# Kernel optimization log

Measured on AMD Instinct MI355X. Metric: run time of the kernel, lower is better.

Reference implementation:

```python
import jax, jax.numpy as jnp
import numpy as np

N, E = 50000, 600000
IN_C, HID, OUT_C = 256, 128, 2
R, B, L = 7, 8, 3
ALPHA = 0.1


def _rgcn(x, src, dst, etype, comp, basis, root, bias):
    # comp: [R,B], basis: [B,d,d] -> per-relation weights W: [R,d,d]
    n, d = x.shape
    W = jnp.einsum('rb,bdf->rdf', comp, basis)
    # combined (dst, relation) segment id for per-relation mean aggregation
    seg = dst * R + etype
    msg = x[src]  # [E,d] gather
    s = jax.ops.segment_sum(msg, seg, num_segments=n * R)  # [N*R,d]
    cnt = jax.ops.segment_sum(jnp.ones((E,), x.dtype), seg, num_segments=n * R)
    agg = (s / jnp.maximum(cnt, 1.0)[:, None]).reshape(n, R, d)  # per-relation mean
    return x @ root + bias + jnp.einsum('nrd,rdf->nf', agg, W)


def setup_inputs() -> dict:
    key = jax.random.key(0)
    ks = jax.random.split(key, 10)
    sc = 0.05
    x = jax.random.normal(ks[0], (N, IN_C), dtype=jnp.float32)
    edge_index = jax.random.randint(ks[1], (2, E), 0, N)
    edge_type = jax.random.randint(ks[2], (E,), 0, R)
    # GPR temp init: alpha*(1-alpha)^k, last entry (1-alpha)^K
    temp = jnp.asarray(ALPHA * (1.0 - ALPHA) ** np.arange(L + 1), dtype=jnp.float32)
    temp = temp.at[-1].set((1.0 - ALPHA) ** L)
    lin1_w = jax.random.normal(ks[3], (IN_C, HID), jnp.float32) * sc
    lin1_b = jnp.zeros((HID,), jnp.float32)
    lin2_w = jax.random.normal(ks[4], (HID, OUT_C), jnp.float32) * sc
    lin2_b = jnp.zeros((OUT_C,), jnp.float32)
    comps = jax.random.normal(ks[5], (L, R, B), jnp.float32) * sc
    bases = jax.random.normal(ks[6], (L, B, HID, HID), jnp.float32) * sc
    roots = jax.random.normal(ks[7], (L, HID, HID), jnp.float32) * sc
    conv_biases = jnp.zeros((L, HID), jnp.float32)
    return dict(x=x, edge_index=edge_index, edge_type=edge_type, temp=temp,
                lin1_w=lin1_w, lin1_b=lin1_b, lin2_w=lin2_w, lin2_b=lin2_b,
                comps=comps, bases=bases, roots=roots, conv_biases=conv_biases)


def reference(x, edge_index, edge_type, temp, lin1_w, lin1_b, lin2_w, lin2_b,
              comps, bases, roots, conv_biases):
    src, dst = edge_index[0], edge_index[1]
    h = x @ lin1_w + lin1_b
    hidden = h * temp[0]
    cur = hidden
    for i in range(L):
        cur = _rgcn(cur, src, dst, edge_type, comps[i], bases[i], roots[i], conv_biases[i])
        if i < L - 1:
            cur = jax.nn.relu(cur)  # dropout p=0.4 is identity in eval mode
        hidden = hidden + temp[i + 1] * cur
    return hidden @ lin2_w + lin2_b
```

## Files before the change

### kernel.cpp

```cpp
#include <hip/hip_runtime.h>
#include <cstdint>


constexpr int N_NODES  = 50000;
constexpr int E_EDGES  = 600000;
constexpr int R_REL    = 7;
constexpr int HID      = 128;
constexpr int IN_C     = 256;
constexpr int L_LAYERS = 3;
constexpr int AGG_COLS = 896;
constexpr int K_CAT    = 1024;
constexpr int SCAN_BLOCKS = (N_NODES + 255) / 256;

#define DEVI __device__ __forceinline__

using short8  = __attribute__((ext_vector_type(8))) short;
using floatx4 = __attribute__((ext_vector_type(4))) float;

DEVI unsigned short f2bf(float f) {
  unsigned u = __float_as_uint(f);
  unsigned r = (u + 0x7FFFu + ((u >> 16) & 1u)) >> 16;
  return (unsigned short)r;
}
DEVI float bf2f(unsigned short h) { return __uint_as_float(((unsigned)h) << 16); }

__global__ __launch_bounds__(256) void cast_x_kernel(
    const float* __restrict__ x, unsigned short* __restrict__ xbf)
{
  int i = blockIdx.x * 256 + threadIdx.x;
  if (i >= N_NODES * IN_C / 4) return;
  float4 v = ((const float4*)x)[i];
  uint2 p;
  p.x = (unsigned)f2bf(v.x) | ((unsigned)f2bf(v.y) << 16);
  p.y = (unsigned)f2bf(v.z) | ((unsigned)f2bf(v.w) << 16);
  ((uint2*)xbf)[i] = p;
}

__global__ __launch_bounds__(256) void cast_w1_kernel(
    const float* __restrict__ w1, unsigned short* __restrict__ w1T)
{
  int t = blockIdx.x * 256 + threadIdx.x;
  if (t >= HID * IN_C) return;
  int m = t >> 8, k = t & 255;
  w1T[m * IN_C + k] = f2bf(w1[k * HID + m]);
}

__global__ __launch_bounds__(256) void build_wcat2(
    const float* __restrict__ comps,
    const float* __restrict__ bases,
    const float* __restrict__ roots,
    unsigned short* __restrict__ wcat2T)
{
  int t = blockIdx.x * 256 + threadIdx.x;
  if (t >= L_LAYERS * 128 * K_CAT) return;
  int l   = t >> 17;
  int rem = t & 131071;
  int f   = rem >> 10;
  int k   = rem & 1023;
  float v;
  if (k < 128) {
    v = roots[((size_t)l * 128 + k) * 128 + f];
  } else {
    int r = (k - 128) >> 7, d = (k - 128) & 127;
    const float* cp = comps + ((size_t)l * R_REL + r) * 8;
    const float* bp = bases + (((size_t)l * 8) * 128 + d) * 128 + f;
    float s = 0.f;
#pragma unroll
    for (int b = 0; b < 8; ++b) s += cp[b] * bp[(size_t)b * 128 * 128];
    v = s;
  }
  wcat2T[t] = f2bf(v);
}

__global__ __launch_bounds__(256) void hist_kernel(
    const int* __restrict__ ei, const int* __restrict__ et,
    int* __restrict__ cntRel, int* __restrict__ cntDst)
{
  int e = blockIdx.x * 256 + threadIdx.x;
  if (e >= E_EDGES) return;
  int dst = ei[E_EDGES + e];
  atomicAdd(&cntRel[dst * R_REL + et[e]], 1);
  atomicAdd(&cntDst[dst], 1);
}

__global__ __launch_bounds__(256) void inv_kernel(float* __restrict__ invc)
{
  int s = blockIdx.x * 256 + threadIdx.x;
  if (s >= N_NODES * R_REL) return;
  int c = ((const int*)invc)[s];
  if (c < 1) c = 1;
  invc[s] = 1.0f / (float)c;
}

__global__ __launch_bounds__(256) void scan1_kernel(
    const int* __restrict__ cntDst, int* __restrict__ tmpOff,
    int* __restrict__ blockSums)
{
  __shared__ int s[256];
  int i = blockIdx.x * 256 + threadIdx.x;
  int v = (i < N_NODES) ? cntDst[i] : 0;
  s[threadIdx.x] = v;
  __syncthreads();
#pragma unroll
  for (int d = 1; d < 256; d <<= 1) {
    int t = (threadIdx.x >= d) ? s[threadIdx.x - d] : 0;
    __syncthreads();
    s[threadIdx.x] += t;
    __syncthreads();
  }
  if (i < N_NODES) tmpOff[i] = s[threadIdx.x] - v;
  if (threadIdx.x == 255) blockSums[blockIdx.x] = s[255];
}

__global__ __launch_bounds__(256) void scan2_kernel(int* __restrict__ blockSums)
{
  __shared__ int s[256];
  int v = (threadIdx.x < SCAN_BLOCKS) ? blockSums[threadIdx.x] : 0;
  s[threadIdx.x] = v;
  __syncthreads();
#pragma unroll
  for (int d = 1; d < 256; d <<= 1) {
    int t = (threadIdx.x >= d) ? s[threadIdx.x - d] : 0;
    __syncthreads();
    s[threadIdx.x] += t;
    __syncthreads();
  }
  if (threadIdx.x < SCAN_BLOCKS) blockSums[threadIdx.x] = s[threadIdx.x] - v;
}

__global__ __launch_bounds__(256) void scan3_kernel(
    const int* __restrict__ tmpOff, const int* __restrict__ blockSums,
    int* __restrict__ dstStart)
{
  int i = blockIdx.x * 256 + threadIdx.x;
  if (i < N_NODES) dstStart[i] = tmpOff[i] + blockSums[blockIdx.x];
  if (i == 0) dstStart[N_NODES] = E_EDGES;
}

__global__ __launch_bounds__(256) void place_kernel(
    const int* __restrict__ ei, const int* __restrict__ et,
    const int* __restrict__ dstStart, int* __restrict__ cursor,
    int* __restrict__ epack)
{
  int e = blockIdx.x * 256 + threadIdx.x;
  if (e >= E_EDGES) return;
  int src = ei[e], dst = ei[E_EDGES + e], r = et[e];
  int pos = dstStart[dst] + atomicAdd(&cursor[dst], 1);
  epack[pos] = src | (r << 16);
}

__global__ __launch_bounds__(256) void agg2_kernel(
    const unsigned short* __restrict__ curA,
    const int* __restrict__ epack,
    const int* __restrict__ dstStart,
    const float* __restrict__ invc,
    unsigned short* __restrict__ aggB)
{
  __shared__ float accF[4][AGG_COLS];
  const int tid  = threadIdx.x;
  const int w    = tid >> 6;
  const int lane = tid & 63;
  const int dst0 = blockIdx.x * 4;
  const int dst  = dst0 + w;

  for (int i = tid; i < 4 * AGG_COLS; i += 256) ((float*)accF)[i] = 0.f;
  __syncthreads();

  int p0 = dstStart[dst], p1 = dstStart[dst + 1];
  for (int p = p0; p < p1; p += 64) {
    int m = p1 - p; if (m > 64) m = 64;
    int pk_l = (lane < m) ? epack[p + lane] : 0;
    for (int i = 0; i < m; ++i) {
      int pk  = __shfl(pk_l, i);
      int src = pk & 0xFFFF;
      int r   = pk >> 16;
      unsigned v = *(const unsigned*)(curA + (size_t)src * HID + lane * 2);
      float2* ap = (float2*)&accF[w][r * HID + lane * 2];
      float2 a = *ap;
      a.x += bf2f((unsigned short)(v & 0xFFFF));
      a.y += bf2f((unsigned short)(v >> 16));
      *ap = a;
    }
  }
  __syncthreads();

  for (int c = tid; c < 4 * (AGG_COLS / 8); c += 256) {
    int dl  = c / 112;
    int cin = c - dl * 112;
    int d0  = cin * 8;
    int r   = d0 >> 7;
    float sc = invc[(dst0 + dl) * R_REL + r];
    const float* ap = &accF[dl][d0];
    uint4 pck;
    pck.x = (unsigned)f2bf(ap[0] * sc) | ((unsigned)f2bf(ap[1] * sc) << 16);
    pck.y = (unsigned)f2bf(ap[2] * sc) | ((unsigned)f2bf(ap[3] * sc) << 16);
    pck.z = (unsigned)f2bf(ap[4] * sc) | ((unsigned)f2bf(ap[5] * sc) << 16);
    pck.w = (unsigned)f2bf(ap[6] * sc) | ((unsigned)f2bf(ap[7] * sc) << 16);
    *(uint4*)(aggB + (size_t)(dst0 + dl) * AGG_COLS + d0) = pck;
  }
}

__global__ __launch_bounds__(256) void gemm_lin1(
    const unsigned short* __restrict__ A,
    const unsigned short* __restrict__ BT,
    const float* __restrict__ bias,
    const float* __restrict__ temp,
    float* __restrict__ out0,
    unsigned short* __restrict__ outT)
{
  __shared__ unsigned short As[128][136];
  __shared__ unsigned short Bs[128][136];
  const int tid  = threadIdx.x;
  const int row0 = blockIdx.x * 128;
  const int lane = tid & 63;
  const int wid  = tid >> 6;
  const int wrow = (wid & 1) * 64;
  const int wcol = (wid >> 1) * 64;
  const int l15  = lane & 15;
  const int quad = lane >> 4;

  floatx4 acc[4][4] = {};

  for (int k0 = 0; k0 < IN_C; k0 += 128) {
#pragma unroll
    for (int it = 0; it < 8; ++it) {
      int chunk = it * 256 + tid;
      int r = chunk >> 4, cc = (chunk & 15) << 3;
      int grow = row0 + r;
      uint4 va = make_uint4(0u, 0u, 0u, 0u);
      if (grow < N_NODES)
        va = *(const uint4*)(A + (size_t)grow * IN_C + k0 + cc);
      *(uint4*)(&As[r][cc]) = va;
      *(uint4*)(&Bs[r][cc]) = *(const uint4*)(BT + (size_t)r * IN_C + k0 + cc);
    }
    __syncthreads();
#pragma unroll
    for (int ks = 0; ks < 4; ++ks) {
      int kc = ks * 32 + quad * 8;
      short8 af[4], bfr[4];
#pragma unroll
      for (int i = 0; i < 4; ++i)
        af[i] = *(const short8*)(&As[wrow + i * 16 + l15][kc]);
#pragma unroll
      for (int j = 0; j < 4; ++j)
        bfr[j] = *(const short8*)(&Bs[wcol + j * 16 + l15][kc]);
#pragma unroll
      for (int i = 0; i < 4; ++i)
#pragma unroll
        for (int j = 0; j < 4; ++j)
          acc[i][j] = __builtin_amdgcn_mfma_f32_16x16x32_bf16(
              af[i], bfr[j], acc[i][j], 0, 0, 0);
    }
    __syncthreads();
  }

  float t0 = temp[0];
#pragma unroll
  for (int i = 0; i < 4; ++i) {
    int lrow0 = wrow + i * 16 + quad * 4;
#pragma unroll
    for (int j = 0; j < 4; ++j) {
      int gcol = wcol + j * 16 + l15;
      float bb = bias[gcol];
#pragma unroll
      for (int r = 0; r < 4; ++r) {
        float v = t0 * (acc[i][j][r] + bb);
        int grow = row0 + lrow0 + r;
        if (grow < N_NODES) out0[(size_t)grow * HID + gcol] = v;
        As[lrow0 + r][gcol] = f2bf(v);
      }
    }
  }
  __syncthreads();
#pragma unroll
  for (int it = 0; it < 8; ++it) {
    int chunk = it * 256 + tid;
    int r = chunk >> 4, cc = (chunk & 15) << 3;
    int grow = row0 + r;
    if (grow < N_NODES)
      *(uint4*)(outT + (size_t)grow * HID + cc) = *(const uint4*)(&As[r][cc]);
  }
}

__global__ __launch_bounds__(256) void gemm_layer(
    const unsigned short* __restrict__ curA,
    const unsigned short* __restrict__ aggB,
    const unsigned short* __restrict__ BT,
    const float* __restrict__ bias,
    float* __restrict__ out0)
{
  __shared__ unsigned short As[128][136];
  __shared__ unsigned short Bs[128][136];
  const int tid  = threadIdx.x;
  const int row0 = blockIdx.x * 128;
  const int lane = tid & 63;
  const int wid  = tid >> 6;
  const int wrow = (wid & 1) * 64;
  const int wcol = (wid >> 1) * 64;
  const int l15  = lane & 15;
  const int quad = lane >> 4;

  floatx4 acc[4][4] = {};

  for (int k0 = 0; k0 < K_CAT; k0 += 128) {
#pragma unroll
    for (int it = 0; it < 8; ++it) {
      int chunk = it * 256 + tid;
      int r = chunk >> 4, cc = (chunk & 15) << 3;
      int grow = row0 + r;
      uint4 va = make_uint4(0u, 0u, 0u, 0u);
      if (grow < N_NODES) {
        if (k0 == 0)
          va = *(const uint4*)(curA + (size_t)grow * HID + cc);
        else
          va = *(const uint4*)(aggB + (size_t)grow * AGG_COLS + (k0 - 128) + cc);
      }
      *(uint4*)(&As[r][cc]) = va;
      *(uint4*)(&Bs[r][cc]) = *(const uint4*)(BT + (size_t)r * K_CAT + k0 + cc);
    }
    __syncthreads();
#pragma unroll
    for (int ks = 0; ks < 4; ++ks) {
      int kc = ks * 32 + quad * 8;
      short8 af[4], bfr[4];
#pragma unroll
      for (int i = 0; i < 4; ++i)
        af[i] = *(const short8*)(&As[wrow + i * 16 + l15][kc]);
#pragma unroll
      for (int j = 0; j < 4; ++j)
        bfr[j] = *(const short8*)(&Bs[wcol + j * 16 + l15][kc]);
#pragma unroll
      for (int i = 0; i < 4; ++i)
#pragma unroll
        for (int j = 0; j < 4; ++j)
          acc[i][j] = __builtin_amdgcn_mfma_f32_16x16x32_bf16(
              af[i], bfr[j], acc[i][j], 0, 0, 0);
    }
    __syncthreads();
  }

#pragma unroll
  for (int i = 0; i < 4; ++i) {
    int lrow0 = wrow + i * 16 + quad * 4;
#pragma unroll
    for (int j = 0; j < 4; ++j) {
      int gcol = wcol + j * 16 + l15;
      float bb = bias[gcol];
#pragma unroll
      for (int r = 0; r < 4; ++r) {
        int grow = row0 + lrow0 + r;
        if (grow < N_NODES)
          out0[(size_t)grow * HID + gcol] = acc[i][j][r] + bb;
      }
    }
  }
}

__global__ __launch_bounds__(256) void epilogue_kernel(
    const float* __restrict__ curB, float* __restrict__ hidden,
    unsigned short* __restrict__ curA, const float* __restrict__ temp, int layer)
{
  int i = blockIdx.x * 256 + threadIdx.x;
  if (i >= N_NODES * HID / 4) return;
  float tl = temp[layer + 1];
  float4 c = ((const float4*)curB)[i];
  if (layer < L_LAYERS - 1) {
    c.x = fmaxf(c.x, 0.f); c.y = fmaxf(c.y, 0.f);
    c.z = fmaxf(c.z, 0.f); c.w = fmaxf(c.w, 0.f);
  }
  float4 h = ((const float4*)hidden)[i];
  h.x += tl * c.x; h.y += tl * c.y; h.z += tl * c.z; h.w += tl * c.w;
  ((float4*)hidden)[i] = h;
  if (layer < L_LAYERS - 1) {
    uint2 p;
    p.x = (unsigned)f2bf(c.x) | ((unsigned)f2bf(c.y) << 16);
    p.y = (unsigned)f2bf(c.z) | ((unsigned)f2bf(c.w) << 16);
    ((uint2*)curA)[i] = p;
  }
}

__global__ __launch_bounds__(256) void final_kernel(
    const float* __restrict__ hidden, const float* __restrict__ w2,
    const float* __restrict__ b2, float* __restrict__ out)
{
  int node = blockIdx.x * 4 + (threadIdx.x >> 6);
  int lane = threadIdx.x & 63;
  if (node >= N_NODES) return;
  float h0 = hidden[(size_t)node * HID + lane];
  float h1 = hidden[(size_t)node * HID + 64 + lane];
  float a0 = h0 * w2[lane * 2 + 0] + h1 * w2[(lane + 64) * 2 + 0];
  float a1 = h0 * w2[lane * 2 + 1] + h1 * w2[(lane + 64) * 2 + 1];
#pragma unroll
  for (int off = 32; off > 0; off >>= 1) {
    a0 += __shfl_down(a0, off);
    a1 += __shfl_down(a1, off);
  }
  if (lane == 0) {
    out[node * 2 + 0] = a0 + b2[0];
    out[node * 2 + 1] = a1 + b2[1];
  }
}

extern "C" void kernel_launch(void* const* d_in, const int* in_sizes, int n_in,
                              void* d_out, int out_size, void* d_ws, size_t ws_size,
                              hipStream_t stream) {
  const float* x     = (const float*)d_in[0];
  const int*   ei    = (const int*)d_in[1];
  const int*   et    = (const int*)d_in[2];
  const float* temp  = (const float*)d_in[3];
  const float* w1    = (const float*)d_in[4];
  const float* b1    = (const float*)d_in[5];
  const float* w2    = (const float*)d_in[6];
  const float* b2    = (const float*)d_in[7];
  const float* comps = (const float*)d_in[8];
  const float* bases = (const float*)d_in[9];
  const float* roots = (const float*)d_in[10];
  const float* cbias = (const float*)d_in[11];

  char* ws = (char*)d_ws;
  size_t off = 0;
  auto take = [&](size_t bytes) {
    char* p = ws + off;
    off = (off + bytes + 255) & ~(size_t)255;
    return p;
  };
  unsigned short* wcat2T = (unsigned short*)take((size_t)L_LAYERS * 128 * K_CAT * 2);
  unsigned short* xbf    = (unsigned short*)take((size_t)N_NODES * IN_C * 2);
  unsigned short* w1T    = (unsigned short*)take((size_t)HID * IN_C * 2);
  float* invc    = (float*)take((size_t)N_NODES * R_REL * 4);
  int*   cntDst  = (int*)take((size_t)N_NODES * 4);
  int*   cursor  = (int*)take((size_t)N_NODES * 4);
  int*   tmpOff  = (int*)take((size_t)N_NODES * 4);
  int*   blockSums = (int*)take((size_t)SCAN_BLOCKS * 4);
  int*   dstStart  = (int*)take((size_t)(N_NODES + 1) * 4);
  int*   epack     = (int*)take((size_t)E_EDGES * 4);
  float* hidden  = (float*)take((size_t)N_NODES * HID * 4);
  unsigned short* curA = (unsigned short*)take((size_t)N_NODES * HID * 2);
  float* curB    = (float*)take((size_t)N_NODES * HID * 4);
  unsigned short* aggB = (unsigned short*)take((size_t)N_NODES * AGG_COLS * 2);

  hipMemsetAsync(invc, 0, (size_t)N_NODES * R_REL * 4, stream);
  hipMemsetAsync(cntDst, 0, (size_t)N_NODES * 4, stream);
  hipMemsetAsync(cursor, 0, (size_t)N_NODES * 4, stream);

  hipLaunchKernelGGL(build_wcat2, dim3((L_LAYERS * 128 * K_CAT + 255) / 256),
                     dim3(256), 0, stream, comps, bases, roots, wcat2T);
  hipLaunchKernelGGL(cast_x_kernel, dim3((N_NODES * IN_C / 4 + 255) / 256),
                     dim3(256), 0, stream, x, xbf);
  hipLaunchKernelGGL(cast_w1_kernel, dim3((HID * IN_C + 255) / 256), dim3(256),
                     0, stream, w1, w1T);
  hipLaunchKernelGGL(hist_kernel, dim3((E_EDGES + 255) / 256), dim3(256), 0,
                     stream, ei, et, (int*)invc, cntDst);
  hipLaunchKernelGGL(inv_kernel, dim3((N_NODES * R_REL + 255) / 256), dim3(256),
                     0, stream, invc);
  hipLaunchKernelGGL(scan1_kernel, dim3(SCAN_BLOCKS), dim3(256), 0, stream,
                     cntDst, tmpOff, blockSums);
  hipLaunchKernelGGL(scan2_kernel, dim3(1), dim3(256), 0, stream, blockSums);
  hipLaunchKernelGGL(scan3_kernel, dim3(SCAN_BLOCKS), dim3(256), 0, stream,
                     tmpOff, blockSums, dstStart);
  hipLaunchKernelGGL(place_kernel, dim3((E_EDGES + 255) / 256), dim3(256), 0,
                     stream, ei, et, dstStart, cursor, epack);

  const int rowBlocks = (N_NODES + 127) / 128;
  hipLaunchKernelGGL(gemm_lin1, dim3(rowBlocks), dim3(256), 0, stream,
                     xbf, w1T, b1, temp, hidden, curA);

  for (int l = 0; l < L_LAYERS; ++l) {
    hipLaunchKernelGGL(agg2_kernel, dim3(N_NODES / 4), dim3(256), 0, stream,
                       curA, epack, dstStart, invc, aggB);
    hipLaunchKernelGGL(gemm_layer, dim3(rowBlocks), dim3(256), 0, stream,
                       curA, aggB, wcat2T + (size_t)l * 128 * K_CAT,
                       cbias + (size_t)l * HID, curB);
    hipLaunchKernelGGL(epilogue_kernel, dim3(N_NODES * HID / 4 / 256), dim3(256),
                       0, stream, curB, hidden, curA, temp, l);
  }

  hipLaunchKernelGGL(final_kernel, dim3((N_NODES + 3) / 4), dim3(256), 0, stream,
                     hidden, w2, b2, (float*)d_out);
}
```

Measured before the change: 591.2 us.

## Sort edges by (dst,relation), slice aggregation by feature columns, fuse epilogue into GEMM

```diff
diff --git a/kernel.cpp b/kernel.cpp
--- a/kernel.cpp
+++ b/kernel.cpp
@@ -10,7 +10,8 @@
 constexpr int L_LAYERS = 3;
 constexpr int AGG_COLS = 896;
 constexpr int K_CAT    = 1024;
-constexpr int SCAN_BLOCKS = (N_NODES + 255) / 256;
+constexpr int NR       = N_NODES * R_REL;
+constexpr int SCANR_BLOCKS = (NR + 255) / 256;
 
 #define DEVI __device__ __forceinline__
 
@@ -74,31 +75,20 @@
 
 __global__ __launch_bounds__(256) void hist_kernel(
     const int* __restrict__ ei, const int* __restrict__ et,
-    int* __restrict__ cntRel, int* __restrict__ cntDst)
+    int* __restrict__ cntRel)
 {
   int e = blockIdx.x * 256 + threadIdx.x;
   if (e >= E_EDGES) return;
-  int dst = ei[E_EDGES + e];
-  atomicAdd(&cntRel[dst * R_REL + et[e]], 1);
-  atomicAdd(&cntDst[dst], 1);
-}
-
-__global__ __launch_bounds__(256) void inv_kernel(float* __restrict__ invc)
-{
-  int s = blockIdx.x * 256 + threadIdx.x;
-  if (s >= N_NODES * R_REL) return;
-  int c = ((const int*)invc)[s];
-  if (c < 1) c = 1;
-  invc[s] = 1.0f / (float)c;
-}
-
-__global__ __launch_bounds__(256) void scan1_kernel(
-    const int* __restrict__ cntDst, int* __restrict__ tmpOff,
+  atomicAdd(&cntRel[ei[E_EDGES + e] * R_REL + et[e]], 1);
+}
+
+__global__ __launch_bounds__(256) void scanA_kernel(
+    const int* __restrict__ cnt, int* __restrict__ tmpOff,
     int* __restrict__ blockSums)
 {
   __shared__ int s[256];
   int i = blockIdx.x * 256 + threadIdx.x;
-  int v = (i < N_NODES) ? cntDst[i] : 0;
+  int v = (i < NR) ? cnt[i] : 0;
   s[threadIdx.x] = v;
   __syncthreads();
 #pragma unroll
@@ -108,95 +98,86 @@
     s[threadIdx.x] += t;
     __syncthreads();
   }
-  if (i < N_NODES) tmpOff[i] = s[threadIdx.x] - v;
+  if (i < NR) tmpOff[i] = s[threadIdx.x] - v;
   if (threadIdx.x == 255) blockSums[blockIdx.x] = s[255];
 }
 
-__global__ __launch_bounds__(256) void scan2_kernel(int* __restrict__ blockSums)
+__global__ __launch_bounds__(256) void scanB_kernel(int* __restrict__ bs)
 {
   __shared__ int s[256];
-  int v = (threadIdx.x < SCAN_BLOCKS) ? blockSums[threadIdx.x] : 0;
-  s[threadIdx.x] = v;
+  __shared__ int carry;
+  if (threadIdx.x == 0) carry = 0;
   __syncthreads();
-#pragma unroll
-  for (int d = 1; d < 256; d <<= 1) {
-    int t = (threadIdx.x >= d) ? s[threadIdx.x - d] : 0;
-    __syncthreads();
-    s[threadIdx.x] += t;
-    __syncthreads();
-  }
-  if (threadIdx.x < SCAN_BLOCKS) blockSums[threadIdx.x] = s[threadIdx.x] - v;
-}
-
-__global__ __launch_bounds__(256) void scan3_kernel(
+  for (int base = 0; base < SCANR_BLOCKS; base += 256) {
+    int cOld = carry;
+    int i = base + threadIdx.x;
+    int v = (i < SCANR_BLOCKS) ? bs[i] : 0;
+    s[threadIdx.x] = v;
+    __syncthreads();
+#pragma unroll
+    for (int d = 1; d < 256; d <<= 1) {
+      int t = (threadIdx.x >= d) ? s[threadIdx.x - d] : 0;
+      __syncthreads();
+      s[threadIdx.x] += t;
+      __syncthreads();
+    }
+    if (i < SCANR_BLOCKS) bs[i] = s[threadIdx.x] - v + cOld;
+    __syncthreads();
+    if (threadIdx.x == 0) carry = cOld + s[255];
+    __syncthreads();
+  }
+}
+
+__global__ __launch_bounds__(256) void scanC_kernel(
     const int* __restrict__ tmpOff, const int* __restrict__ blockSums,
-    int* __restrict__ dstStart)
+    int* __restrict__ drs)
 {
   int i = blockIdx.x * 256 + threadIdx.x;
-  if (i < N_NODES) dstStart[i] = tmpOff[i] + blockSums[blockIdx.x];
-  if (i == 0) dstStart[N_NODES] = E_EDGES;
+  if (i < NR) drs[i] = tmpOff[i] + blockSums[blockIdx.x];
+  if (i == 0) drs[NR] = E_EDGES;
 }
 
 __global__ __launch_bounds__(256) void place_kernel(
     const int* __restrict__ ei, const int* __restrict__ et,
-    const int* __restrict__ dstStart, int* __restrict__ cursor,
-    int* __restrict__ epack)
+    const int* __restrict__ drs, int* __restrict__ cursor,
+    unsigned short* __restrict__ esrc)
 {
   int e = blockIdx.x * 256 + threadIdx.x;
   if (e >= E_EDGES) return;
-  int src = ei[e], dst = ei[E_EDGES + e], r = et[e];
-  int pos = dstStart[dst] + atomicAdd(&cursor[dst], 1);
-  epack[pos] = src | (r << 16);
-}
-
-__global__ __launch_bounds__(256) void agg2_kernel(
+  int seg = ei[E_EDGES + e] * R_REL + et[e];
+  int pos = drs[seg] + atomicAdd(&cursor[seg], 1);
+  esrc[pos] = (unsigned short)ei[e];
+}
+
+__global__ __launch_bounds__(256) void agg_slice_kernel(
     const unsigned short* __restrict__ curA,
-    const int* __restrict__ epack,
-    const int* __restrict__ dstStart,
-    const float* __restrict__ invc,
+    const unsigned short* __restrict__ esrc,
+    const int* __restrict__ drs,
     unsigned short* __restrict__ aggB)
 {
-  __shared__ float accF[4][AGG_COLS];
-  const int tid  = threadIdx.x;
-  const int w    = tid >> 6;
-  const int lane = tid & 63;
-  const int dst0 = blockIdx.x * 4;
-  const int dst  = dst0 + w;
-
-  for (int i = tid; i < 4 * AGG_COLS; i += 256) ((float*)accF)[i] = 0.f;
-  __syncthreads();
-
-  int p0 = dstStart[dst], p1 = dstStart[dst + 1];
-  for (int p = p0; p < p1; p += 64) {
-    int m = p1 - p; if (m > 64) m = 64;
-    int pk_l = (lane < m) ? epack[p + lane] : 0;
-    for (int i = 0; i < m; ++i) {
-      int pk  = __shfl(pk_l, i);
-      int src = pk & 0xFFFF;
-      int r   = pk >> 16;
-      unsigned v = *(const unsigned*)(curA + (size_t)src * HID + lane * 2);
-      float2* ap = (float2*)&accF[w][r * HID + lane * 2];
-      float2 a = *ap;
-      a.x += bf2f((unsigned short)(v & 0xFFFF));
-      a.y += bf2f((unsigned short)(v >> 16));
-      *ap = a;
-    }
-  }
-  __syncthreads();
-
-  for (int c = tid; c < 4 * (AGG_COLS / 8); c += 256) {
-    int dl  = c / 112;
-    int cin = c - dl * 112;
-    int d0  = cin * 8;
-    int r   = d0 >> 7;
-    float sc = invc[(dst0 + dl) * R_REL + r];
-    const float* ap = &accF[dl][d0];
-    uint4 pck;
-    pck.x = (unsigned)f2bf(ap[0] * sc) | ((unsigned)f2bf(ap[1] * sc) << 16);
-    pck.y = (unsigned)f2bf(ap[2] * sc) | ((unsigned)f2bf(ap[3] * sc) << 16);
-    pck.z = (unsigned)f2bf(ap[4] * sc) | ((unsigned)f2bf(ap[5] * sc) << 16);
-    pck.w = (unsigned)f2bf(ap[6] * sc) | ((unsigned)f2bf(ap[7] * sc) << 16);
-    *(uint4*)(aggB + (size_t)(dst0 + dl) * AGG_COLS + d0) = pck;
+  const int slice = blockIdx.x;
+  const int tid   = threadIdx.x;
+  const int dl    = tid >> 3;
+  const int pr    = tid & 7;
+  const int dst   = blockIdx.y * 32 + dl;
+  if (dst >= N_NODES) return;
+  const int dim0 = slice * 16 + pr * 2;
+  const unsigned* colp = (const unsigned*)(curA + dim0);
+
+  int a = drs[dst * R_REL];
+#pragma unroll
+  for (int r = 0; r < R_REL; ++r) {
+    int b = drs[dst * R_REL + r + 1];
+    float sx = 0.f, sy = 0.f;
+    for (int p = a; p < b; ++p) {
+      unsigned v = colp[(int)esrc[p] * 64];
+      sx += bf2f((unsigned short)(v & 0xFFFF));
+      sy += bf2f((unsigned short)(v >> 16));
+    }
+    float sc = (b > a) ? 1.0f / (float)(b - a) : 0.f;
+    unsigned pck = (unsigned)f2bf(sx * sc) | ((unsigned)f2bf(sy * sc) << 16);
+    *(unsigned*)(aggB + (size_t)dst * AGG_COLS + r * HID + dim0) = pck;
+    a = b;
   }
 }
 
@@ -287,7 +268,10 @@
     const unsigned short* __restrict__ aggB,
     const unsigned short* __restrict__ BT,
     const float* __restrict__ bias,
-    float* __restrict__ out0)
+    const float* __restrict__ temp,
+    float* __restrict__ hidden,
+    unsigned short* __restrict__ curAout,
+    int layer)
 {
   __shared__ unsigned short As[128][136];
   __shared__ unsigned short Bs[128][136];
@@ -339,6 +323,8 @@
     __syncthreads();
   }
 
+  const float tl = temp[layer + 1];
+  const bool isLast = (layer == L_LAYERS - 1);
 #pragma unroll
   for (int i = 0; i < 4; ++i) {
     int lrow0 = wrow + i * 16 + quad * 4;
@@ -349,33 +335,26 @@
 #pragma unroll
       for (int r = 0; r < 4; ++r) {
         int grow = row0 + lrow0 + r;
-        if (grow < N_NODES)
-          out0[(size_t)grow * HID + gcol] = acc[i][j][r] + bb;
+        float c = acc[i][j][r] + bb;
+        if (!isLast) c = fmaxf(c, 0.f);
+        if (grow < N_NODES) {
+          float* hp = hidden + (size_t)grow * HID + gcol;
+          *hp += tl * c;
+        }
+        As[lrow0 + r][gcol] = f2bf(c);
       }
     }
   }
-}
-
-__global__ __launch_bounds__(256) void epilogue_kernel(
-    const float* __restrict__ curB, float* __restrict__ hidden,
-    unsigned short* __restrict__ curA, const float* __restrict__ temp, int layer)
-{
-  int i = blockIdx.x * 256 + threadIdx.x;
-  if (i >= N_NODES * HID / 4) return;
-  float tl = temp[layer + 1];
-  float4 c = ((const float4*)curB)[i];
-  if (layer < L_LAYERS - 1) {
-    c.x = fmaxf(c.x, 0.f); c.y = fmaxf(c.y, 0.f);
-    c.z = fmaxf(c.z, 0.f); c.w = fmaxf(c.w, 0.f);
-  }
-  float4 h = ((const float4*)hidden)[i];
-  h.x += tl * c.x; h.y += tl * c.y; h.z += tl * c.z; h.w += tl * c.w;
-  ((float4*)hidden)[i] = h;
-  if (layer < L_LAYERS - 1) {
-    uint2 p;
-    p.x = (unsigned)f2bf(c.x) | ((unsigned)f2bf(c.y) << 16);
-    p.y = (unsigned)f2bf(c.z) | ((unsigned)f2bf(c.w) << 16);
-    ((uint2*)curA)[i] = p;
+  if (!isLast) {
+    __syncthreads();
+#pragma unroll
+    for (int it = 0; it < 8; ++it) {
+      int chunk = it * 256 + tid;
+      int r = chunk >> 4, cc = (chunk & 15) << 3;
+      int grow = row0 + r;
+      if (grow < N_NODES)
+        *(uint4*)(curAout + (size_t)grow * HID + cc) = *(const uint4*)(&As[r][cc]);
+    }
   }
 }
 
@@ -427,21 +406,19 @@
   unsigned short* wcat2T = (unsigned short*)take((size_t)L_LAYERS * 128 * K_CAT * 2);
   unsigned short* xbf    = (unsigned short*)take((size_t)N_NODES * IN_C * 2);
   unsigned short* w1T    = (unsigned short*)take((size_t)HID * IN_C * 2);
-  float* invc    = (float*)take((size_t)N_NODES * R_REL * 4);
-  int*   cntDst  = (int*)take((size_t)N_NODES * 4);
-  int*   cursor  = (int*)take((size_t)N_NODES * 4);
-  int*   tmpOff  = (int*)take((size_t)N_NODES * 4);
-  int*   blockSums = (int*)take((size_t)SCAN_BLOCKS * 4);
-  int*   dstStart  = (int*)take((size_t)(N_NODES + 1) * 4);
-  int*   epack     = (int*)take((size_t)E_EDGES * 4);
+  int*   cntRel  = (int*)take((size_t)NR * 4);
+  int*   tmpOffR = (int*)take((size_t)NR * 4);
+  int*   blockSumsR = (int*)take((size_t)SCANR_BLOCKS * 4);
+  int*   drs     = (int*)take((size_t)(NR + 1) * 4);
+  int*   cursorR = (int*)take((size_t)NR * 4);
+  unsigned short* esrc = (unsigned short*)take((size_t)E_EDGES * 2);
   float* hidden  = (float*)take((size_t)N_NODES * HID * 4);
-  unsigned short* curA = (unsigned short*)take((size_t)N_NODES * HID * 2);
-  float* curB    = (float*)take((size_t)N_NODES * HID * 4);
-  unsigned short* aggB = (unsigned short*)take((size_t)N_NODES * AGG_COLS * 2);
-
-  hipMemsetAsync(invc, 0, (size_t)N_NODES * R_REL * 4, stream);
-  hipMemsetAsync(cntDst, 0, (size_t)N_NODES * 4, stream);
-  hipMemsetAsync(cursor, 0, (size_t)N_NODES * 4, stream);
+  unsigned short* curA  = (unsigned short*)take((size_t)N_NODES * HID * 2);
+  unsigned short* curA2 = (unsigned short*)take((size_t)N_NODES * HID * 2);
+  unsigned short* aggB  = (unsigned short*)take((size_t)N_NODES * AGG_COLS * 2);
+
+  hipMemsetAsync(cntRel, 0, (size_t)NR * 4, stream);
+  hipMemsetAsync(cursorR, 0, (size_t)NR * 4, stream);
 
   hipLaunchKernelGGL(build_wcat2, dim3((L_LAYERS * 128 * K_CAT + 255) / 256),
                      dim3(256), 0, stream, comps, bases, roots, wcat2T);
@@ -450,29 +427,28 @@
   hipLaunchKernelGGL(cast_w1_kernel, dim3((HID * IN_C + 255) / 256), dim3(256),
                      0, stream, w1, w1T);
   hipLaunchKernelGGL(hist_kernel, dim3((E_EDGES + 255) / 256), dim3(256), 0,
-                     stream, ei, et, (int*)invc, cntDst);
-  hipLaunchKernelGGL(inv_kernel, dim3((N_NODES * R_REL + 255) / 256), dim3(256),
-                     0, stream, invc);
-  hipLaunchKernelGGL(scan1_kernel, dim3(SCAN_BLOCKS), dim3(256), 0, stream,
-                     cntDst, tmpOff, blockSums);
-  hipLaunchKernelGGL(scan2_kernel, dim3(1), dim3(256), 0, stream, blockSums);
-  hipLaunchKernelGGL(scan3_kernel, dim3(SCAN_BLOCKS), dim3(256), 0, stream,
-                     tmpOff, blockSums, dstStart);
+                     stream, ei, et, cntRel);
+  hipLaunchKernelGGL(scanA_kernel, dim3(SCANR_BLOCKS), dim3(256), 0, stream,
+                     cntRel, tmpOffR, blockSumsR);
+  hipLaunchKernelGGL(scanB_kernel, dim3(1), dim3(256), 0, stream, blockSumsR);
+  hipLaunchKernelGGL(scanC_kernel, dim3(SCANR_BLOCKS), dim3(256), 0, stream,
+                     tmpOffR, blockSumsR, drs);
   hipLaunchKernelGGL(place_kernel, dim3((E_EDGES + 255) / 256), dim3(256), 0,
-                     stream, ei, et, dstStart, cursor, epack);
+                     stream, ei, et, drs, cursorR, esrc);
 
   const int rowBlocks = (N_NODES + 127) / 128;
   hipLaunchKernelGGL(gemm_lin1, dim3(rowBlocks), dim3(256), 0, stream,
                      xbf, w1T, b1, temp, hidden, curA);
 
+  const unsigned short* cin = curA;
+  unsigned short* cout = curA2;
   for (int l = 0; l < L_LAYERS; ++l) {
-    hipLaunchKernelGGL(agg2_kernel, dim3(N_NODES / 4), dim3(256), 0, stream,
-                       curA, epack, dstStart, invc, aggB);
+    hipLaunchKernelGGL(agg_slice_kernel, dim3(8, (N_NODES + 31) / 32), dim3(256),
+                       0, stream, cin, esrc, drs, aggB);
     hipLaunchKernelGGL(gemm_layer, dim3(rowBlocks), dim3(256), 0, stream,
-                       curA, aggB, wcat2T + (size_t)l * 128 * K_CAT,
-                       cbias + (size_t)l * HID, curB);
-    hipLaunchKernelGGL(epilogue_kernel, dim3(N_NODES * HID / 4 / 256), dim3(256),
-                       0, stream, curB, hidden, curA, temp, l);
+                       cin, aggB, wcat2T + (size_t)l * 128 * K_CAT,
+                       cbias + (size_t)l * HID, temp, hidden, cout, l);
+    const unsigned short* t = cin; cin = cout; cout = (unsigned short*)t;
   }
 
   hipLaunchKernelGGL(final_kernel, dim3((N_NODES + 3) / 4), dim3(256), 0, stream,
```

Result: slower. 815.1 us (+37.9%).
